# Kernel optimization log

Hardware: AMD Instinct MI355X
Metric: run time of the kernel (lower is better)

## Reference

```python
import jax, jax.numpy as jnp
import numpy as np

NHO, NFO = 400000, 100000
EHO, EFO, EBI = 4000000, 2000000, 800000
NUM_CLASSES = 10


def _gcn_conv(x, W, b, src, dst, w, n):
    # PyG GCNConv with edge weights + default self-loops (weight 1):
    # deg[i] = sum_{e: dst(e)=i} w_e + 1 ; norm_e = d^{-1/2}[src] * w_e * d^{-1/2}[dst]
    deg = jax.ops.segment_sum(w, dst, num_segments=n) + 1.0
    dinv = jax.lax.rsqrt(deg)
    xw = x @ W                                    # [n, out]
    coef = dinv[src] * w * dinv[dst]              # [E]
    agg = jax.ops.segment_sum(xw[src] * coef[:, None], dst, num_segments=n)
    # self-loop contribution: dinv[i]*1*dinv[i] = 1/deg[i]
    return agg + xw * (dinv * dinv)[:, None] + b


def setup_inputs() -> dict:
    key = jax.random.key(0)
    ks = jax.random.split(key, 24)
    def lin(i, fin, fout, s=None):
        s = 1.0 / np.sqrt(fin) if s is None else s
        return jax.random.uniform(ks[i], (fin, fout), jnp.float32, -s, s)
    inp = {
        'x_ho': jax.random.normal(ks[0], (NHO, 60), jnp.float32),
        'x_fo': jax.random.normal(ks[1], (NFO, 32), jnp.float32),
        'ho_src': jax.random.randint(ks[2], (EHO,), 0, NHO, jnp.int32),
        'ho_dst': jax.random.randint(ks[3], (EHO,), 0, NHO, jnp.int32),
        'ho_w': jax.random.uniform(ks[4], (EHO,), jnp.float32),
        'fo_src': jax.random.randint(ks[5], (EFO,), 0, NFO, jnp.int32),
        'fo_dst': jax.random.randint(ks[6], (EFO,), 0, NFO, jnp.int32),
        'fo_w': jax.random.uniform(ks[7], (EFO,), jnp.float32),
        'bi_src': jax.random.randint(ks[8], (EBI,), 0, NHO, jnp.int32),
        'bi_dst': jax.random.randint(ks[9], (EBI,), 0, NFO, jnp.int32),
        'num_ho_nodes': NHO,
        'num_fo_nodes': NFO,
        # GCNConv params (weight [in,out], bias [out])
        'W220': lin(10, 60, 16), 'b220': jnp.zeros((16,), jnp.float32),
        'W221': lin(11, 16, 32), 'b221': jnp.zeros((32,), jnp.float32),
        'W110': lin(12, 32, 16), 'b110': jnp.zeros((16,), jnp.float32),
        'W111': lin(13, 16, 32), 'b111': jnp.zeros((32,), jnp.float32),
        # BipartiteGraphOperator linears
        'lin1_w': lin(14, 32, 32), 'lin1_b': jax.random.uniform(ks[15], (32,), jnp.float32, -0.17, 0.17),
        'lin2_w': lin(16, 32, 32), 'lin2_b': jax.random.uniform(ks[17], (32,), jnp.float32, -0.17, 0.17),
        # output MLP
        'mlp_w': lin(18, 32, NUM_CLASSES), 'mlp_b': jnp.zeros((NUM_CLASSES,), jnp.float32),
    }
    return inp


def reference(x_ho, x_fo, ho_src, ho_dst, ho_w, fo_src, fo_dst, fo_w,
              bi_src, bi_dst, num_ho_nodes, num_fo_nodes,
              W220, b220, W221, b221, W110, b110, W111, b111,
              lin1_w, lin1_b, lin2_w, lin2_b, mlp_w, mlp_b):
    elu = jax.nn.elu
    # dropout is identity in eval mode
    # HO branch (GCN stack on higher-order graph)
    h = elu(_gcn_conv(x_ho, W220, b220, ho_src, ho_dst, ho_w, num_ho_nodes))
    h = elu(_gcn_conv(h, W221, b221, ho_src, ho_dst, ho_w, num_ho_nodes))
    # FO branch (GCN stack on first-order graph)
    h1 = elu(_gcn_conv(x_fo, W110, b110, fo_src, fo_dst, fo_w, num_fo_nodes))
    h1 = elu(_gcn_conv(h1, W111, b111, fo_src, fo_dst, fo_w, num_fo_nodes))
    # Bipartite operator: default MessagePassing message is x_j (source side),
    # aggregated 'add' at targets; lin2(h1) is computed but unused by default semantics.
    m = h @ lin1_w + lin1_b                              # [NHO, 32]
    _unused = h1 @ lin2_w + lin2_b                       # faithful to original (dead value)
    agg = jax.ops.segment_sum(m[bi_src], bi_dst, num_segments=num_fo_nodes)  # [NFO, 32]
    out = elu(agg)
    return out @ mlp_w + mlp_b                           # [NFO, num_classes]
```

## Files before the change

kernel.cpp:

```cpp
#include <hip/hip_runtime.h>
#include <math.h>

#define SCAN_BLOCK 1024
#define BK_BITS 9
#define BKSZ 512
#define CH 16384
#define FXS 33554432.0f

static __device__ __forceinline__ float elu_f(float x) {
    return x > 0.0f ? x : expm1f(x);
}


__global__ __launch_bounds__(256) void k_passA(
    const int* __restrict__ hd, int* __restrict__ counts, int nChunks, int Eho, int NB,
    const int* __restrict__ bd, int* __restrict__ cntBI, unsigned short* __restrict__ rankBI,
    int Ebi, int biB,
    const float* __restrict__ x, const float* __restrict__ W, float* __restrict__ Axw, int N)
{
    __shared__ float smem[64 * 61 + 960];
    int bid = blockIdx.x;
    if (bid < nChunks) {
        unsigned* h = (unsigned*)smem;
        for (int t = threadIdx.x; t < NB; t += 256) h[t] = 0u;
        __syncthreads();
        int e0 = bid * CH;
        int e1 = e0 + CH; if (e1 > Eho) e1 = Eho;
        for (int e = e0 + threadIdx.x; e < e1; e += 256)
            atomicAdd(&h[(unsigned)hd[e] >> BK_BITS], 1u);
        __syncthreads();
        for (int t = threadIdx.x; t < NB; t += 256)
            counts[(size_t)t * nChunks + bid] = (int)h[t];
        return;
    }
    bid -= nChunks;
    if (bid < biB) {
        int i = bid * 256 + threadIdx.x;
        int stride = biB * 256;
        for (; i < Ebi; i += stride)
            rankBI[i] = (unsigned short)atomicAdd(&cntBI[bd[i]], 1);
        return;
    }
    bid -= biB;
    float* sx = smem;
    float* sW = smem + 64 * 61;
    for (int t = threadIdx.x; t < 960; t += 256) sW[t] = W[t];
    int base = bid * 64;
    int rows = N - base; if (rows > 64) rows = 64;
    const float4* xg = (const float4*)(x + (size_t)base * 60);
    int nf4 = rows * 15;
    for (int j = threadIdx.x; j < nf4; j += 256) {
        float4 v = xg[j];
        int r = j / 15, k4 = j - r * 15;
        float* dst = &sx[r * 61 + k4 * 4];
        dst[0] = v.x; dst[1] = v.y; dst[2] = v.z; dst[3] = v.w;
    }
    __syncthreads();
    int t = threadIdx.x;
    if (t < rows) {
        const float* xr = &sx[t * 61];
        float acc[16];
        #pragma unroll
        for (int o = 0; o < 16; o++) acc[o] = 0.0f;
        #pragma unroll
        for (int k = 0; k < 60; k++) {
            float xv = xr[k];
            #pragma unroll
            for (int o = 0; o < 16; o++) acc[o] = fmaf(xv, sW[k * 16 + o], acc[o]);
        }
        float4* yr = (float4*)(Axw + (size_t)(base + t) * 16);
        yr[0] = make_float4(acc[0], acc[1], acc[2], acc[3]);
        yr[1] = make_float4(acc[4], acc[5], acc[6], acc[7]);
        yr[2] = make_float4(acc[8], acc[9], acc[10], acc[11]);
        yr[3] = make_float4(acc[12], acc[13], acc[14], acc[15]);
    }
}


__global__ void k_scan2(const int* __restrict__ in1, int* __restrict__ out1, int n1, int nb1,
                        const int* __restrict__ in2, int* __restrict__ out2, int n2,
                        int* __restrict__ sums1, int* __restrict__ sums2) {
    __shared__ int tmp[SCAN_BLOCK];
    int b = blockIdx.x;
    const int* in; int* out; int n; int* sums; int bb;
    if (b < nb1) { in = in1; out = out1; n = n1; sums = sums1; bb = b; }
    else         { in = in2; out = out2; n = n2; sums = sums2; bb = b - nb1; }
    int gid = bb * SCAN_BLOCK + threadIdx.x;
    int v = (gid < n) ? in[gid] : 0;
    tmp[threadIdx.x] = v;
    __syncthreads();
    for (int off = 1; off < SCAN_BLOCK; off <<= 1) {
        int t = (threadIdx.x >= off) ? tmp[threadIdx.x - off] : 0;
        __syncthreads();
        tmp[threadIdx.x] += t;
        __syncthreads();
    }
    if (gid < n) out[gid] = tmp[threadIdx.x] - v;
    if (threadIdx.x == SCAN_BLOCK - 1) sums[bb] = tmp[threadIdx.x];
}

__global__ void k_scan_sums2(int* __restrict__ sums1, int nb1,
                             int* __restrict__ sums2, int nb2) {
    __shared__ int tmp[SCAN_BLOCK];
    int* s = (blockIdx.x == 0) ? sums1 : sums2;
    int nb = (blockIdx.x == 0) ? nb1 : nb2;
    int v = (threadIdx.x < nb) ? s[threadIdx.x] : 0;
    tmp[threadIdx.x] = v;
    __syncthreads();
    for (int off = 1; off < SCAN_BLOCK; off <<= 1) {
        int t = (threadIdx.x >= off) ? tmp[threadIdx.x - off] : 0;
        __syncthreads();
        tmp[threadIdx.x] += t;
        __syncthreads();
    }
    if (threadIdx.x < nb) s[threadIdx.x] = tmp[threadIdx.x] - v;
}

__global__ void k_scan_add2(int* __restrict__ out1, const int* __restrict__ sums1,
                            int n1, int tot1, int nb1,
                            int* __restrict__ out2, const int* __restrict__ sums2,
                            int n2, int tot2) {
    int b = blockIdx.x;
    if (b < nb1) {
        int gid = b * SCAN_BLOCK + threadIdx.x;
        if (gid < n1) out1[gid] += sums1[b];
        if (gid == 0) out1[n1] = tot1;
    } else {
        int b2 = b - nb1;
        int gid = b2 * SCAN_BLOCK + threadIdx.x;
        if (gid < n2) out2[gid] += sums2[b2];
        if (gid == 0) out2[n2] = tot2;
    }
}


__global__ __launch_bounds__(256) void k_passC(
    const int* __restrict__ hs, const int* __restrict__ hd, const float* __restrict__ hw,
    const int* __restrict__ countsS, int nChunks, int NB, int Eho,
    int2* __restrict__ eS,
    const int* __restrict__ bs, const int* __restrict__ bd,
    const unsigned short* __restrict__ rankBI, const int* __restrict__ rsbi,
    int* __restrict__ srcbi, int Ebi)
{
    __shared__ int cur[1024];
    int bid = blockIdx.x;
    if (bid < nChunks) {
        for (int t = threadIdx.x; t < NB; t += 256)
            cur[t] = countsS[(size_t)t * nChunks + bid];
        __syncthreads();
        int e0 = bid * CH;
        int e1 = e0 + CH; if (e1 > Eho) e1 = Eho;
        for (int e = e0 + threadIdx.x; e < e1; e += 256) {
            int d = hd[e];
            int pos = atomicAdd(&cur[(unsigned)d >> BK_BITS], 1);
            eS[pos] = make_int2(hs[e] | ((d & (BKSZ - 1)) << 19), __float_as_int(hw[e]));
        }
        return;
    }
    bid -= nChunks;
    int i = bid * 256 + threadIdx.x;
    int stride = ((int)gridDim.x - nChunks) * 256;
    for (; i < Ebi; i += stride)
        srcbi[rsbi[bd[i]] + rankBI[i]] = bs[i];
}


__global__ __launch_bounds__(1024) void k_passD(
    const int2* __restrict__ eS, const int* __restrict__ countsS, int nChunks,
    int NB, int Eho, int NHO,
    int2* __restrict__ pairs, int* __restrict__ rs_ho, float* __restrict__ dinv)
{
    __shared__ unsigned cnt[BKSZ];
    __shared__ unsigned fx[BKSZ];
    __shared__ int sc[BKSZ];
    __shared__ int cur[BKSZ];
    int b = blockIdx.x;
    int base = countsS[(size_t)b * nChunks];
    int end  = (b == NB - 1) ? Eho : countsS[(size_t)(b + 1) * nChunks];
    int tid = threadIdx.x;
    if (tid < BKSZ) { cnt[tid] = 0u; fx[tid] = 0u; }
    __syncthreads();
    for (int e = base + tid; e < end; e += 1024) {
        int2 p = eS[e];
        int n = (unsigned)p.x >> 19;
        atomicAdd(&cnt[n], 1u);
        atomicAdd(&fx[n], (unsigned)(__int_as_float(p.y) * FXS + 0.5f));
    }
    __syncthreads();
    if (tid < BKSZ) sc[tid] = (int)cnt[tid];
    __syncthreads();
    for (int off = 1; off < BKSZ; off <<= 1) {
        int t = (tid < BKSZ && tid >= off) ? sc[tid - off] : 0;
        __syncthreads();
        if (tid < BKSZ) sc[tid] += t;
        __syncthreads();
    }
    if (tid < BKSZ) {
        int gn = b * BKSZ + tid;
        if (gn < NHO) {
            int off0 = sc[tid] - (int)cnt[tid];
            cur[tid] = base + off0;
            rs_ho[gn] = base + off0;
            dinv[gn] = rsqrtf((float)fx[tid] * (1.0f / FXS) + 1.0f);
        }
    }
    if (b == NB - 1 && tid == 0) rs_ho[NHO] = Eho;
    __syncthreads();
    for (int e = base + tid; e < end; e += 1024) {
        int2 p = eS[e];
        int n = (unsigned)p.x >> 19;
        int pos = atomicAdd(&cur[n], 1);
        pairs[pos] = make_int2(p.x & 0x7FFFF, p.y);
    }
}


__global__ void k_passE(int2* __restrict__ pairs, const float* __restrict__ dinv, int E) {
    int i = blockIdx.x * blockDim.x + threadIdx.x;
    int stride = gridDim.x * blockDim.x;
    for (; i < E; i += stride) {
        int2 p = pairs[i];
        pairs[i] = make_int2(p.x, __float_as_int(__int_as_float(p.y) * dinv[p.x]));
    }
}

#define EDGE_FMA(SRCTAB, J) \
    acc = fmaf(__int_as_float(__shfl(p.y, (J), 16)), \
               SRCTAB[(size_t)__shfl(p.x, (J), 16) * 16 + ln], acc);


__global__ void k_gather1(const int2* __restrict__ pairs, const int* __restrict__ rs,
                          const float* __restrict__ dinv, const float* __restrict__ A,
                          const float* __restrict__ b, float* __restrict__ B, int N) {
    int t = blockIdx.x * blockDim.x + threadIdx.x;
    int node = t >> 4, ln = t & 15;
    if (node >= N) return;
    int beg = rs[node], end = rs[node + 1];
    float acc = 0.0f;
    for (int k = beg; k < end; k += 16) {
        int take = end - k; if (take > 16) take = 16;
        int2 p = pairs[k + (ln < take ? ln : take - 1)];
        if (take == 16) {
            #pragma unroll
            for (int j = 0; j < 16; j++) { EDGE_FMA(A, j) }
        } else {
            int j = 0;
            if (take >= 8) {
                #pragma unroll
                for (int jj = 0; jj < 8; jj++) { EDGE_FMA(A, jj) }
                j = 8;
            }
            if (take - j >= 4) {
                #pragma unroll
                for (int jj = 0; jj < 4; jj++) { EDGE_FMA(A, j + jj) }
                j += 4;
            }
            for (; j < take; j++) { EDGE_FMA(A, j) }
        }
    }
    float di = dinv[node];
    float v = fmaf(di, acc, fmaf(A[(size_t)node * 16 + ln], di * di, b[ln]));
    B[(size_t)node * 16 + ln] = elu_f(v);
}


__global__ void k_gather2(const int2* __restrict__ pairs, const int* __restrict__ rs,
                          const float* __restrict__ dinv, const float* __restrict__ B,
                          const float* __restrict__ W221, const float* __restrict__ b221,
                          const float* __restrict__ L1w, const float* __restrict__ L1b,
                          float* __restrict__ M, int N) {
    __shared__ float sW[16 * 32];
    __shared__ float sb2[32];
    __shared__ float sL[32 * 32];
    __shared__ float sLb[32];
    for (int t = threadIdx.x; t < 512; t += blockDim.x) sW[t] = W221[t];
    for (int t = threadIdx.x; t < 1024; t += blockDim.x) sL[t] = L1w[t];
    if (threadIdx.x < 32) { sb2[threadIdx.x] = b221[threadIdx.x]; sLb[threadIdx.x] = L1b[threadIdx.x]; }
    __syncthreads();
    int t = blockIdx.x * blockDim.x + threadIdx.x;
    int node = t >> 4, ln = t & 15;
    if (node >= N) return;
    int beg = rs[node], end = rs[node + 1];
    float acc = 0.0f;
    for (int k = beg; k < end; k += 16) {
        int take = end - k; if (take > 16) take = 16;
        int2 p = pairs[k + (ln < take ? ln : take - 1)];
        if (take == 16) {
            #pragma unroll
            for (int j = 0; j < 16; j++) { EDGE_FMA(B, j) }
        } else {
            int j = 0;
            if (take >= 8) {
                #pragma unroll
                for (int jj = 0; jj < 8; jj++) { EDGE_FMA(B, jj) }
                j = 8;
            }
            if (take - j >= 4) {
                #pragma unroll
                for (int jj = 0; jj < 4; jj++) { EDGE_FMA(B, j + jj) }
                j += 4;
            }
            for (; j < take; j++) { EDGE_FMA(B, j) }
        }
    }
    float di = dinv[node];
    float agg = fmaf(di, acc, B[(size_t)node * 16 + ln] * di * di);
    float h2a = sb2[ln], h2b = sb2[ln + 16];
    #pragma unroll
    for (int k = 0; k < 16; k++) {
        float ak = __shfl(agg, k, 16);
        h2a += ak * sW[k * 32 + ln];
        h2b += ak * sW[k * 32 + ln + 16];
    }
    h2a = elu_f(h2a); h2b = elu_f(h2b);
    float m0 = sLb[ln], m1 = sLb[ln + 16];
    #pragma unroll
    for (int k = 0; k < 16; k++) {
        float a0 = __shfl(h2a, k, 16);
        float a1 = __shfl(h2b, k, 16);
        m0 += a0 * sL[k * 32 + ln]        + a1 * sL[(k + 16) * 32 + ln];
        m1 += a0 * sL[k * 32 + ln + 16]   + a1 * sL[(k + 16) * 32 + ln + 16];
    }
    float* mr = M + (size_t)node * 32;
    mr[ln] = m0; mr[ln + 16] = m1;
}


__global__ void k_bi_mlp(const int* __restrict__ srcs, const int* __restrict__ rs,
                         const float* __restrict__ M, const float* __restrict__ mw,
                         const float* __restrict__ mb, float* __restrict__ out, int N) {
    __shared__ float sW[32 * 10];
    __shared__ float sb[10];
    for (int t = threadIdx.x; t < 320; t += blockDim.x) sW[t] = mw[t];
    if (threadIdx.x < 10) sb[threadIdx.x] = mb[threadIdx.x];
    __syncthreads();
    int t = blockIdx.x * blockDim.x + threadIdx.x;
    int node = t >> 5, ln = t & 31;
    if (node >= N) return;
    int beg = rs[node], end = rs[node + 1];
    float acc = 0.0f;
    for (int k = beg; k < end; k += 32) {
        int take = end - k; if (take > 32) take = 32;
        int ms = srcs[k + (ln < take ? ln : take - 1)];
        if (take == 32) {
            #pragma unroll
            for (int j = 0; j < 32; j++)
                acc += M[(size_t)__shfl(ms, j, 32) * 32 + ln];
        } else {
            int j = 0;
            if (take >= 16) {
                #pragma unroll
                for (int jj = 0; jj < 16; jj++)
                    acc += M[(size_t)__shfl(ms, jj, 32) * 32 + ln];
                j = 16;
            }
            if (take - j >= 8) {
                #pragma unroll
                for (int jj = 0; jj < 8; jj++)
                    acc += M[(size_t)__shfl(ms, j + jj, 32) * 32 + ln];
                j += 8;
            }
            if (take - j >= 4) {
                #pragma unroll
                for (int jj = 0; jj < 4; jj++)
                    acc += M[(size_t)__shfl(ms, j + jj, 32) * 32 + ln];
                j += 4;
            }
            for (; j < take; j++)
                acc += M[(size_t)__shfl(ms, j, 32) * 32 + ln];
        }
    }
    float e = elu_f(acc);
    int lw = ln < 10 ? ln : 0;
    float o = ln < 10 ? sb[ln] : 0.0f;
    #pragma unroll
    for (int k = 0; k < 32; k++) {
        float ak = __shfl(e, k, 32);
        o += ak * sW[k * 10 + lw];
    }
    if (ln < 10) out[(size_t)node * 10 + ln] = o;
}


extern "C" void kernel_launch(void* const* d_in, const int* in_sizes, int n_in,
                              void* d_out, int out_size, void* d_ws, size_t ws_size,
                              hipStream_t stream) {
    const float* x_ho   = (const float*)d_in[0];
    const int*   ho_src = (const int*)d_in[2];
    const int*   ho_dst = (const int*)d_in[3];
    const float* ho_w   = (const float*)d_in[4];
    const int*   bi_src = (const int*)d_in[8];
    const int*   bi_dst = (const int*)d_in[9];
    const float* W220   = (const float*)d_in[12];
    const float* b220   = (const float*)d_in[13];
    const float* W221   = (const float*)d_in[14];
    const float* b221   = (const float*)d_in[15];
    const float* lin1_w = (const float*)d_in[20];
    const float* lin1_b = (const float*)d_in[21];
    const float* mlp_w  = (const float*)d_in[24];
    const float* mlp_b  = (const float*)d_in[25];

    const int NHO = in_sizes[0] / 60;
    const int EHO = in_sizes[2];
    const int EBI = in_sizes[8];
    const int NFO = out_size / 10;
    float* out = (float*)d_out;

    const int NB = (NHO + BKSZ - 1) / BKSZ;
    const int nChunks = (EHO + CH - 1) / CH;
    const int NC = NB * nChunks;
    const int biB = 2048;
    const int xwB = (NHO + 63) / 64;

    size_t off = 0;
    float* ws = (float*)d_ws;
    int2*  pairs = (int2*)(ws + off); off += (size_t)2 * EHO;
    size_t uWords = (size_t)2 * EHO;
    if ((size_t)16 * NHO > uWords) uWords = (size_t)16 * NHO;
    int2*  eS = (int2*)(ws + off);
    float* B  = (float*)(ws + off); off += uWords;
    float* A  = ws + off; off += (size_t)32 * NHO;
    float* M  = A;
    float* dinv  = ws + off; off += NHO;
    int*   rs_ho = (int*)(ws + off); off += NHO + 1;
    int*   counts  = (int*)(ws + off); off += NC;
    int*   countsS = (int*)(ws + off); off += NC + 1;
    int*   cntBI = (int*)(ws + off); off += NFO;
    int*   rs_bi = (int*)(ws + off); off += NFO + 1;
    int*   srcbi = (int*)(ws + off); off += EBI;
    unsigned short* rankBI = (unsigned short*)(ws + off); off += (EBI + 1) / 2;
    int*   sums1 = (int*)(ws + off); off += SCAN_BLOCK;
    int*   sums2 = (int*)(ws + off); off += SCAN_BLOCK;

    const int BLK = 256;
    const int nb1 = (NC + SCAN_BLOCK - 1) / SCAN_BLOCK;
    const int nb2 = (NFO + SCAN_BLOCK - 1) / SCAN_BLOCK;

    hipMemsetAsync(cntBI, 0, (size_t)NFO * 4, stream);

    k_passA<<<nChunks + biB + xwB, BLK, 0, stream>>>(
        ho_dst, counts, nChunks, EHO, NB,
        bi_dst, cntBI, rankBI, EBI, biB,
        x_ho, W220, A, NHO);

    k_scan2<<<nb1 + nb2, SCAN_BLOCK, 0, stream>>>(
        counts, countsS, NC, nb1, cntBI, rs_bi, NFO, sums1, sums2);
    k_scan_sums2<<<2, SCAN_BLOCK, 0, stream>>>(sums1, nb1, sums2, nb2);
    k_scan_add2<<<nb1 + nb2, SCAN_BLOCK, 0, stream>>>(
        countsS, sums1, NC, EHO, nb1, rs_bi, sums2, NFO, EBI);

    k_passC<<<nChunks + 2048, BLK, 0, stream>>>(
        ho_src, ho_dst, ho_w, countsS, nChunks, NB, EHO, eS,
        bi_src, bi_dst, rankBI, rs_bi, srcbi, EBI);

    k_passD<<<NB, SCAN_BLOCK, 0, stream>>>(
        eS, countsS, nChunks, NB, EHO, NHO, pairs, rs_ho, dinv);

    {
        long long b = ((long long)EHO + BLK - 1) / BLK;
        k_passE<<<(int)(b > 4096 ? 4096 : b), BLK, 0, stream>>>(pairs, dinv, EHO);
    }

    {
        long long t = (long long)NHO * 16;
        k_gather1<<<(int)((t + BLK - 1) / BLK), BLK, 0, stream>>>(
            pairs, rs_ho, dinv, A, b220, B, NHO);
    }
    {
        long long t = (long long)NHO * 16;
        k_gather2<<<(int)((t + BLK - 1) / BLK), BLK, 0, stream>>>(
            pairs, rs_ho, dinv, B, W221, b221, lin1_w, lin1_b, M, NHO);
    }
    {
        long long t = (long long)NFO * 32;
        k_bi_mlp<<<(int)((t + BLK - 1) / BLK), BLK, 0, stream>>>(
            srcbi, rs_bi, M, mlp_w, mlp_b, out, NFO);
    }
}
```

Before: 509.4 us.

## Store node features in fp16 and fold source-side normalization into features

```diff
diff --git a/kernel.cpp b/kernel.cpp
--- a/kernel.cpp
+++ b/kernel.cpp
@@ -1,4 +1,5 @@
 #include <hip/hip_runtime.h>
+#include <hip/hip_fp16.h>
 #include <math.h>
 
 #define SCAN_BLOCK 1024
@@ -16,7 +17,7 @@
     const int* __restrict__ hd, int* __restrict__ counts, int nChunks, int Eho, int NB,
     const int* __restrict__ bd, int* __restrict__ cntBI, unsigned short* __restrict__ rankBI,
     int Ebi, int biB,
-    const float* __restrict__ x, const float* __restrict__ W, float* __restrict__ Axw, int N)
+    const float* __restrict__ x, const float* __restrict__ W, __half* __restrict__ Axw, int N)
 {
     __shared__ float smem[64 * 61 + 960];
     int bid = blockIdx.x;
@@ -68,11 +69,12 @@
             #pragma unroll
             for (int o = 0; o < 16; o++) acc[o] = fmaf(xv, sW[k * 16 + o], acc[o]);
         }
-        float4* yr = (float4*)(Axw + (size_t)(base + t) * 16);
-        yr[0] = make_float4(acc[0], acc[1], acc[2], acc[3]);
-        yr[1] = make_float4(acc[4], acc[5], acc[6], acc[7]);
-        yr[2] = make_float4(acc[8], acc[9], acc[10], acc[11]);
-        yr[3] = make_float4(acc[12], acc[13], acc[14], acc[15]);
+        __half2 hh[8];
+        #pragma unroll
+        for (int j = 0; j < 8; j++) hh[j] = __floats2half2_rn(acc[2 * j], acc[2 * j + 1]);
+        uint4* yr = (uint4*)(Axw + (size_t)(base + t) * 16);
+        yr[0] = *(uint4*)&hh[0];
+        yr[1] = *(uint4*)&hh[4];
     }
 }
 
@@ -168,12 +170,14 @@
 __global__ __launch_bounds__(1024) void k_passD(
     const int2* __restrict__ eS, const int* __restrict__ countsS, int nChunks,
     int NB, int Eho, int NHO,
-    int2* __restrict__ pairs, int* __restrict__ rs_ho, float* __restrict__ dinv)
+    int2* __restrict__ pairs, int* __restrict__ rs_ho, float* __restrict__ dinv,
+    __half* __restrict__ Ah)
 {
     __shared__ unsigned cnt[BKSZ];
     __shared__ unsigned fx[BKSZ];
     __shared__ int sc[BKSZ];
     __shared__ int cur[BKSZ];
+    __shared__ float sdinv[BKSZ];
     int b = blockIdx.x;
     int base = countsS[(size_t)b * nChunks];
     int end  = (b == NB - 1) ? Eho : countsS[(size_t)(b + 1) * nChunks];
@@ -195,13 +199,17 @@
         if (tid < BKSZ) sc[tid] += t;
         __syncthreads();
     }
+    int gbase = b * BKSZ;
+    int nn = NHO - gbase; if (nn > BKSZ) nn = BKSZ;
     if (tid < BKSZ) {
-        int gn = b * BKSZ + tid;
+        int gn = gbase + tid;
         if (gn < NHO) {
             int off0 = sc[tid] - (int)cnt[tid];
             cur[tid] = base + off0;
             rs_ho[gn] = base + off0;
-            dinv[gn] = rsqrtf((float)fx[tid] * (1.0f / FXS) + 1.0f);
+            float di = rsqrtf((float)fx[tid] * (1.0f / FXS) + 1.0f);
+            dinv[gn] = di;
+            sdinv[tid] = di;
         }
     }
     if (b == NB - 1 && tid == 0) rs_ho[NHO] = Eho;
@@ -212,63 +220,37 @@
         int pos = atomicAdd(&cur[n], 1);
         pairs[pos] = make_int2(p.x & 0x7FFFF, p.y);
     }
-}
-
-
-__global__ void k_passE(int2* __restrict__ pairs, const float* __restrict__ dinv, int E) {
-    int i = blockIdx.x * blockDim.x + threadIdx.x;
-    int stride = gridDim.x * blockDim.x;
-    for (; i < E; i += stride) {
-        int2 p = pairs[i];
-        pairs[i] = make_int2(p.x, __float_as_int(__int_as_float(p.y) * dinv[p.x]));
-    }
-}
-
-#define EDGE_FMA(SRCTAB, J) \
-    acc = fmaf(__int_as_float(__shfl(p.y, (J), 16)), \
-               SRCTAB[(size_t)__shfl(p.x, (J), 16) * 16 + ln], acc);
+    for (int idx = tid; idx < nn * 16; idx += 1024) {
+        int n = idx >> 4;
+        size_t a = (size_t)(gbase + n) * 16 + (idx & 15);
+        Ah[a] = __float2half_rn(__half2float(Ah[a]) * sdinv[n]);
+    }
+}
 
 
 __global__ void k_gather1(const int2* __restrict__ pairs, const int* __restrict__ rs,
-                          const float* __restrict__ dinv, const float* __restrict__ A,
-                          const float* __restrict__ b, float* __restrict__ B, int N) {
+                          const float* __restrict__ dinv, const __half* __restrict__ A,
+                          const float* __restrict__ b, __half* __restrict__ B, int N) {
     int t = blockIdx.x * blockDim.x + threadIdx.x;
     int node = t >> 4, ln = t & 15;
     if (node >= N) return;
     int beg = rs[node], end = rs[node + 1];
     float acc = 0.0f;
-    for (int k = beg; k < end; k += 16) {
-        int take = end - k; if (take > 16) take = 16;
-        int2 p = pairs[k + (ln < take ? ln : take - 1)];
-        if (take == 16) {
-            #pragma unroll
-            for (int j = 0; j < 16; j++) { EDGE_FMA(A, j) }
-        } else {
-            int j = 0;
-            if (take >= 8) {
-                #pragma unroll
-                for (int jj = 0; jj < 8; jj++) { EDGE_FMA(A, jj) }
-                j = 8;
-            }
-            if (take - j >= 4) {
-                #pragma unroll
-                for (int jj = 0; jj < 4; jj++) { EDGE_FMA(A, j + jj) }
-                j += 4;
-            }
-            for (; j < take; j++) { EDGE_FMA(A, j) }
-        }
+    for (int k = beg; k < end; k++) {
+        int2 p = pairs[k];
+        acc = fmaf(__int_as_float(p.y), __half2float(A[(size_t)p.x * 16 + ln]), acc);
     }
     float di = dinv[node];
-    float v = fmaf(di, acc, fmaf(A[(size_t)node * 16 + ln], di * di, b[ln]));
-    B[(size_t)node * 16 + ln] = elu_f(v);
+    float v = fmaf(di, acc + __half2float(A[(size_t)node * 16 + ln]), b[ln]);
+    B[(size_t)node * 16 + ln] = __float2half_rn(di * elu_f(v));
 }
 
 
 __global__ void k_gather2(const int2* __restrict__ pairs, const int* __restrict__ rs,
-                          const float* __restrict__ dinv, const float* __restrict__ B,
+                          const float* __restrict__ dinv, const __half* __restrict__ B,
                           const float* __restrict__ W221, const float* __restrict__ b221,
                           const float* __restrict__ L1w, const float* __restrict__ L1b,
-                          float* __restrict__ M, int N) {
+                          __half* __restrict__ M, int N) {
     __shared__ float sW[16 * 32];
     __shared__ float sb2[32];
     __shared__ float sL[32 * 32];
@@ -282,29 +264,12 @@
     if (node >= N) return;
     int beg = rs[node], end = rs[node + 1];
     float acc = 0.0f;
-    for (int k = beg; k < end; k += 16) {
-        int take = end - k; if (take > 16) take = 16;
-        int2 p = pairs[k + (ln < take ? ln : take - 1)];
-        if (take == 16) {
-            #pragma unroll
-            for (int j = 0; j < 16; j++) { EDGE_FMA(B, j) }
-        } else {
-            int j = 0;
-            if (take >= 8) {
-                #pragma unroll
-                for (int jj = 0; jj < 8; jj++) { EDGE_FMA(B, jj) }
-                j = 8;
-            }
-            if (take - j >= 4) {
-                #pragma unroll
-                for (int jj = 0; jj < 4; jj++) { EDGE_FMA(B, j + jj) }
-                j += 4;
-            }
-            for (; j < take; j++) { EDGE_FMA(B, j) }
-        }
+    for (int k = beg; k < end; k++) {
+        int2 p = pairs[k];
+        acc = fmaf(__int_as_float(p.y), __half2float(B[(size_t)p.x * 16 + ln]), acc);
     }
     float di = dinv[node];
-    float agg = fmaf(di, acc, B[(size_t)node * 16 + ln] * di * di);
+    float agg = di * (acc + __half2float(B[(size_t)node * 16 + ln]));
     float h2a = sb2[ln], h2b = sb2[ln + 16];
     #pragma unroll
     for (int k = 0; k < 16; k++) {
@@ -321,13 +286,13 @@
         m0 += a0 * sL[k * 32 + ln]        + a1 * sL[(k + 16) * 32 + ln];
         m1 += a0 * sL[k * 32 + ln + 16]   + a1 * sL[(k + 16) * 32 + ln + 16];
     }
-    float* mr = M + (size_t)node * 32;
-    mr[ln] = m0; mr[ln + 16] = m1;
+    __half* mr = M + (size_t)node * 32;
+    mr[ln] = __float2half_rn(m0); mr[ln + 16] = __float2half_rn(m1);
 }
 
 
 __global__ void k_bi_mlp(const int* __restrict__ srcs, const int* __restrict__ rs,
-                         const float* __restrict__ M, const float* __restrict__ mw,
+                         const __half* __restrict__ M, const float* __restrict__ mw,
                          const float* __restrict__ mb, float* __restrict__ out, int N) {
     __shared__ float sW[32 * 10];
     __shared__ float sb[10];
@@ -339,37 +304,8 @@
     if (node >= N) return;
     int beg = rs[node], end = rs[node + 1];
     float acc = 0.0f;
-    for (int k = beg; k < end; k += 32) {
-        int take = end - k; if (take > 32) take = 32;
-        int ms = srcs[k + (ln < take ? ln : take - 1)];
-        if (take == 32) {
-            #pragma unroll
-            for (int j = 0; j < 32; j++)
-                acc += M[(size_t)__shfl(ms, j, 32) * 32 + ln];
-        } else {
-            int j = 0;
-            if (take >= 16) {
-                #pragma unroll
-                for (int jj = 0; jj < 16; jj++)
-                    acc += M[(size_t)__shfl(ms, jj, 32) * 32 + ln];
-                j = 16;
-            }
-            if (take - j >= 8) {
-                #pragma unroll
-                for (int jj = 0; jj < 8; jj++)
-                    acc += M[(size_t)__shfl(ms, j + jj, 32) * 32 + ln];
-                j += 8;
-            }
-            if (take - j >= 4) {
-                #pragma unroll
-                for (int jj = 0; jj < 4; jj++)
-                    acc += M[(size_t)__shfl(ms, j + jj, 32) * 32 + ln];
-                j += 4;
-            }
-            for (; j < take; j++)
-                acc += M[(size_t)__shfl(ms, j, 32) * 32 + ln];
-        }
-    }
+    for (int k = beg; k < end; k++)
+        acc += __half2float(M[(size_t)srcs[k] * 32 + ln]);
     float e = elu_f(acc);
     int lw = ln < 10 ? ln : 0;
     float o = ln < 10 ? sb[ln] : 0.0f;
@@ -416,11 +352,11 @@
     float* ws = (float*)d_ws;
     int2*  pairs = (int2*)(ws + off); off += (size_t)2 * EHO;
     size_t uWords = (size_t)2 * EHO;
-    if ((size_t)16 * NHO > uWords) uWords = (size_t)16 * NHO;
-    int2*  eS = (int2*)(ws + off);
-    float* B  = (float*)(ws + off); off += uWords;
-    float* A  = ws + off; off += (size_t)32 * NHO;
-    float* M  = A;
+    if ((size_t)8 * NHO > uWords) uWords = (size_t)8 * NHO;
+    int2*   eS = (int2*)(ws + off);
+    __half* B  = (__half*)(ws + off); off += uWords;
+    __half* A  = (__half*)(ws + off); off += (size_t)16 * NHO;
+    __half* M  = A;
     float* dinv  = ws + off; off += NHO;
     int*   rs_ho = (int*)(ws + off); off += NHO + 1;
     int*   counts  = (int*)(ws + off); off += NC;
@@ -454,12 +390,7 @@
         bi_src, bi_dst, rankBI, rs_bi, srcbi, EBI);
 
     k_passD<<<NB, SCAN_BLOCK, 0, stream>>>(
-        eS, countsS, nChunks, NB, EHO, NHO, pairs, rs_ho, dinv);
-
-    {
-        long long b = ((long long)EHO + BLK - 1) / BLK;
-        k_passE<<<(int)(b > 4096 ? 4096 : b), BLK, 0, stream>>>(pairs, dinv, EHO);
-    }
+        eS, countsS, nChunks, NB, EHO, NHO, pairs, rs_ho, dinv, A);
 
     {
         long long t = (long long)NHO * 16;
```

Result: slower. 589.4 us (+15.7%).
